# Performance work log

Hardware: AMD Instinct MI355X
Metric: run time of the kernel (lower is better)

Reference implementation:

```python
import jax, jax.numpy as jnp
import numpy as np

N = 50000
E = 800000
D = 128
NEG_SLOPE = 0.2


def _gat_layer(x, W, al, ar, b, src, dst):
    """Single-head DGL-style GATConv with ReLU activation."""
    z = x @ W                                    # [N, D] projected features
    el = z @ al                                  # [N] left attention logits
    er = z @ ar                                  # [N] right attention logits
    e = jax.nn.leaky_relu(el[src] + er[dst], NEG_SLOPE)   # [E]
    # softmax over incoming edges per destination node (numerically stable)
    m = jax.ops.segment_max(e, dst, num_segments=N)       # [N]
    ex = jnp.exp(e - m[dst])                               # [E]
    s = jax.ops.segment_sum(ex, dst, num_segments=N)       # [N]
    alpha = ex / s[dst]                                    # [E]
    out = jax.ops.segment_sum(alpha[:, None] * z[src], dst, num_segments=N)  # [N, D]
    return jax.nn.relu(out + b)


def setup_inputs() -> dict:
    key = jax.random.key(0)
    ks = jax.random.split(key, 16)
    s = 0.05
    inp = {
        "f": jax.random.normal(ks[0], (N, D), dtype=jnp.float32),
        "src": jax.random.randint(ks[1], (E,), 0, N, dtype=jnp.int32),
        "dst": jax.random.randint(ks[2], (E,), 0, N, dtype=jnp.int32),
    }
    for i, kb in zip((1, 2, 3), (3, 7, 11)):
        inp[f"W{i}"] = jax.random.normal(ks[kb], (D, D), dtype=jnp.float32) * s
        inp[f"al{i}"] = jax.random.normal(ks[kb + 1], (D,), dtype=jnp.float32) * s
        inp[f"ar{i}"] = jax.random.normal(ks[kb + 2], (D,), dtype=jnp.float32) * s
        inp[f"b{i}"] = jnp.zeros((D,), dtype=jnp.float32)
    return inp


def reference(f, src, dst, W1, al1, ar1, b1, W2, al2, ar2, b2, W3, al3, ar3, b3):
    h = _gat_layer(f, W1, al1, ar1, b1, src, dst)
    h = _gat_layer(h, W2, al2, ar2, b2, src, dst)
    h = _gat_layer(h, W3, al3, ar3, b3, src, dst)
    return h  # [N, D] (single head already squeezed)
```

## Files before the change

kernel.cpp:

```cpp
#include <hip/hip_runtime.h>
#include <hip/hip_fp16.h>
#include <math.h>

#define NN 50000
#define NE 800000
#define DD 128
#define NEG_SLOPE 0.2f
#define CAP 64
#define GBLK ((NN + 63) / 64)
#define WSBLK (3 * 16384 / 256)
#define HBLK ((NE + 255) / 256)
#define SBLK ((NE + 511) / 512)

typedef short frag8 __attribute__((ext_vector_type(8)));
typedef float f32x4 __attribute__((ext_vector_type(4)));

__device__ __forceinline__ unsigned bf16_rne(float x) {
  unsigned u = __float_as_uint(x);
  return (u + 0x7FFFu + ((u >> 16) & 1u)) >> 16;
}

__device__ __forceinline__ void wsplit_body(
    int bid, const float* __restrict__ W0, const float* __restrict__ W1,
    const float* __restrict__ W2, short* __restrict__ Wh, short* __restrict__ Wl) {
  int gidx = bid * 256 + threadIdx.x;
  int L = gidx >> 14;
  int idx = gidx & 16383;
  const float* W = (L == 0) ? W0 : (L == 1) ? W1 : W2;
  int j = idx & 7;
  int lane = (idx >> 3) & 63;
  int tile = idx >> 9;
  int nt = tile & 7, kt = tile >> 3;
  int k = kt * 32 + (lane >> 4) * 8 + j;
  int n = nt * 16 + (lane & 15);
  float x = W[k * DD + n];
  unsigned hu = bf16_rne(x);
  float hf = __uint_as_float(hu << 16);
  unsigned lu = bf16_rne(x - hf);
  Wh[gidx] = (short)hu;
  Wl[gidx] = (short)lu;
}

__device__ __forceinline__ void hist_body(int bid, const int* __restrict__ dst,
                                          int* __restrict__ deg,
                                          unsigned short* __restrict__ edge_slot) {
  int i = bid * 256 + threadIdx.x;
  if (i < NE) edge_slot[i] = (unsigned short)atomicAdd(&deg[dst[i]], 1);
}

__global__ __launch_bounds__(256) void fused_pre(
    const float* __restrict__ W0, const float* __restrict__ W1, const float* __restrict__ W2,
    short* __restrict__ Wh, short* __restrict__ Wl,
    const int* __restrict__ dst, int* __restrict__ deg,
    unsigned short* __restrict__ edge_slot) {
  if (blockIdx.x < WSBLK) wsplit_body(blockIdx.x, W0, W1, W2, Wh, Wl);
  else hist_body(blockIdx.x - WSBLK, dst, deg, edge_slot);
}

__device__ __forceinline__ void gemm_body(
    int bid, short (*sB)[8192], float (*elp)[64], float (*erp)[64],
    const float* __restrict__ x, const short* __restrict__ Wh, const short* __restrict__ Wl,
    const float* __restrict__ al, const float* __restrict__ ar,
    __half* __restrict__ z, float* __restrict__ el, float* __restrict__ er) {
  const int t = threadIdx.x;
  const int w = t >> 6, lane = t & 63;
  const int m = lane & 15, quad = lane >> 4;
  const int half = w >> 2, mw = w & 3;
  const int ntb = half * 4;
  const int R0 = bid * 64 + mw * 16;

  auto stage = [&](int kt, int buf) {
    const uint4* gh = (const uint4*)(Wh + kt * 4096);
    const uint4* gl = (const uint4*)(Wl + kt * 4096);
    uint4* s = (uint4*)sB[buf];
    s[t] = gh[t];
    s[t + 512] = gl[t];
  };

  f32x4 acc[4];
#pragma unroll
  for (int n = 0; n < 4; n++) acc[n] = (f32x4)(0.f);

  int rA = R0 + m; if (rA > NN - 1) rA = NN - 1;

  stage(0, 0);
  __syncthreads();

#pragma unroll
  for (int kt = 0; kt < 4; kt++) {
    const int buf = kt & 1;
    if (kt < 3) stage(kt + 1, buf ^ 1);

    const float* xp = x + (size_t)rA * DD + kt * 32 + quad * 8;
    float xv[8];
    *(float4*)(xv) = *(const float4*)xp;
    *(float4*)(xv + 4) = *(const float4*)(xp + 4);
    frag8 ah, alo;
#pragma unroll
    for (int j = 0; j < 8; j++) {
      unsigned hu = bf16_rne(xv[j]);
      float hf = __uint_as_float(hu << 16);
      ah[j] = (short)hu;
      alo[j] = (short)bf16_rne(xv[j] - hf);
    }
#pragma unroll
    for (int n = 0; n < 4; n++) {
      frag8 bh = *(const frag8*)&sB[buf][(ntb + n) * 512 + lane * 8];
      frag8 bl = *(const frag8*)&sB[buf][4096 + (ntb + n) * 512 + lane * 8];
      acc[n] = __builtin_amdgcn_mfma_f32_16x16x32_bf16(alo, bh, acc[n], 0, 0, 0);
      acc[n] = __builtin_amdgcn_mfma_f32_16x16x32_bf16(ah, bl, acc[n], 0, 0, 0);
      acc[n] = __builtin_amdgcn_mfma_f32_16x16x32_bf16(ah, bh, acc[n], 0, 0, 0);
    }
    __syncthreads();
  }

  float alv[4], arv[4];
#pragma unroll
  for (int n = 0; n < 4; n++) {
    alv[n] = al[(ntb + n) * 16 + m];
    arv[n] = ar[(ntb + n) * 16 + m];
  }
#pragma unroll
  for (int r = 0; r < 4; r++) {
    float pl = 0.f, pr = 0.f;
#pragma unroll
    for (int n = 0; n < 4; n++) { pl += acc[n][r] * alv[n]; pr += acc[n][r] * arv[n]; }
#pragma unroll
    for (int off = 8; off; off >>= 1) {
      pl += __shfl_xor(pl, off, 64);
      pr += __shfl_xor(pr, off, 64);
    }
    int lrow = mw * 16 + quad * 4 + r;
    if (m == 0) { elp[half][lrow] = pl; erp[half][lrow] = pr; }
    int row = R0 + quad * 4 + r;
    if (row < NN) {
#pragma unroll
      for (int n = 0; n < 4; n++) {
        unsigned short hu = __half_as_ushort(__float2half(acc[n][r]));
        unsigned short hn = (unsigned short)__shfl_xor((int)hu, 1, 64);
        if ((m & 1) == 0) {
          __half2 pair = __halves2half2(__ushort_as_half(hu), __ushort_as_half(hn));
          *(__half2*)(z + (size_t)row * DD + (ntb + n) * 16 + m) = pair;
        }
      }
    }
  }
  __syncthreads();
  if (t < 64) {
    int row = bid * 64 + t;
    if (row < NN) {
      el[row] = elp[0][t] + elp[1][t];
      er[row] = erp[0][t] + erp[1][t];
    }
  }
}

__device__ __forceinline__ void scatter_body(
    int bid, const int* __restrict__ src, const int* __restrict__ dst,
    const unsigned short* __restrict__ edge_slot, unsigned short* __restrict__ csr_src) {
  int i = bid * 512 + threadIdx.x;
  if (i >= NE) return;
  int slot = edge_slot[i]; if (slot > CAP - 1) slot = CAP - 1;
  csr_src[dst[i] * CAP + slot] = (unsigned short)src[i];
}

__global__ __launch_bounds__(512) void gemm_mfma(
    const float* __restrict__ x, const short* __restrict__ Wh, const short* __restrict__ Wl,
    const float* __restrict__ al, const float* __restrict__ ar,
    __half* __restrict__ z, float* __restrict__ el, float* __restrict__ er) {
  __shared__ __align__(16) short sB[2][8192];
  __shared__ float elp[2][64], erp[2][64];
  gemm_body(blockIdx.x, sB, elp, erp, x, Wh, Wl, al, ar, z, el, er);
}

__global__ __launch_bounds__(512) void fused_scatter_gemm(
    const float* __restrict__ x, const short* __restrict__ Wh, const short* __restrict__ Wl,
    const float* __restrict__ al, const float* __restrict__ ar,
    __half* __restrict__ z, float* __restrict__ el, float* __restrict__ er,
    const int* __restrict__ src, const int* __restrict__ dst,
    const unsigned short* __restrict__ edge_slot, unsigned short* __restrict__ csr_src) {
  __shared__ __align__(16) short sB[2][8192];
  __shared__ float elp[2][64], erp[2][64];
  if (blockIdx.x < GBLK) gemm_body(blockIdx.x, sB, elp, erp, x, Wh, Wl, al, ar, z, el, er);
  else scatter_body(blockIdx.x - GBLK, src, dst, edge_slot, csr_src);
}

__global__ __launch_bounds__(256) void gat_agg(
    const int* __restrict__ deg, const unsigned short* __restrict__ csr_src,
    const float* __restrict__ el, const float* __restrict__ er,
    const __half* __restrict__ z, const float* __restrict__ b,
    float* __restrict__ out) {
  int node = (int)((blockIdx.x * 256 + threadIdx.x) >> 6);
  int lane = threadIdx.x & 63;
  if (node >= NN) return;
  int dn = deg[node]; if (dn > CAP) dn = CAP;
  int beg = node * CAP;
  float erd = er[node];
  const __half2* zb = (const __half2*)z + lane;

  int sn = 0; float wv = 0.f;
  if (lane < dn) {
    sn = csr_src[beg + lane];
    float e = el[sn] + erd;
    e = (e > 0.f) ? e : NEG_SLOPE * e;
    wv = __expf(e);
  }
  float ssum = wv;

  float2 acc = make_float2(0.f, 0.f);
  for (int jj = 0; jj < dn; jj += 8) {
    float ww[8]; int ss[8];
#pragma unroll
    for (int u = 0; u < 8; u++) {
      ww[u] = __shfl(wv, jj + u, 64);
      ss[u] = __shfl(sn, jj + u, 64);
    }
    float2 zv[8];
#pragma unroll
    for (int u = 0; u < 8; u++) zv[u] = __half22float2(zb[(size_t)ss[u] * 64]);
#pragma unroll
    for (int u = 0; u < 8; u++) { acc.x += ww[u] * zv[u].x; acc.y += ww[u] * zv[u].y; }
  }
#pragma unroll
  for (int off = 32; off; off >>= 1) ssum += __shfl_xor(ssum, off, 64);
  float inv_s = (dn > 0) ? 1.f / ssum : 0.f;

  float2 bv = *(const float2*)(b + lane * 2);
  float ox = fmaxf(acc.x * inv_s + bv.x, 0.f);
  float oy = fmaxf(acc.y * inv_s + bv.y, 0.f);
  *(float2*)(out + (size_t)node * DD + lane * 2) = make_float2(ox, oy);
}

extern "C" void kernel_launch(void* const* d_in, const int* in_sizes, int n_in,
                              void* d_out, int out_size, void* d_ws, size_t ws_size,
                              hipStream_t stream) {
  const float* f   = (const float*)d_in[0];
  const int*   src = (const int*)d_in[1];
  const int*   dst = (const int*)d_in[2];
  const float* W[3]  = {(const float*)d_in[3], (const float*)d_in[7],  (const float*)d_in[11]};
  const float* al[3] = {(const float*)d_in[4], (const float*)d_in[8],  (const float*)d_in[12]};
  const float* ar[3] = {(const float*)d_in[5], (const float*)d_in[9],  (const float*)d_in[13]};
  const float* bb[3] = {(const float*)d_in[6], (const float*)d_in[10], (const float*)d_in[14]};

  short* Wh3 = (short*)d_ws;
  short* Wl3 = Wh3 + 3 * 16384;
  __half* zbuf = (__half*)(Wl3 + 3 * 16384);
  float* hbuf = (float*)(zbuf + (size_t)NN * DD);
  float* el = hbuf + (size_t)NN * DD;
  float* er = el + NN;
  int* deg = (int*)(er + NN);
  unsigned short* edge_slot = (unsigned short*)(deg + NN);
  unsigned short* csr_src   = edge_slot + NE;

  hipMemsetAsync(deg, 0, NN * sizeof(int), stream);
  fused_pre<<<WSBLK + HBLK, 256, 0, stream>>>(W[0], W[1], W[2], Wh3, Wl3, dst, deg, edge_slot);
  fused_scatter_gemm<<<GBLK + SBLK, 512, 0, stream>>>(f, Wh3, Wl3, al[0], ar[0],
                                                      zbuf, el, er,
                                                      src, dst, edge_slot, csr_src);
  gat_agg<<<(NN * 64) / 256, 256, 0, stream>>>(deg, csr_src, el, er, zbuf, bb[0], hbuf);

  gemm_mfma<<<GBLK, 512, 0, stream>>>(hbuf, Wh3 + 16384, Wl3 + 16384,
                                      al[1], ar[1], zbuf, el, er);
  gat_agg<<<(NN * 64) / 256, 256, 0, stream>>>(deg, csr_src, el, er, zbuf, bb[1], hbuf);

  gemm_mfma<<<GBLK, 512, 0, stream>>>(hbuf, Wh3 + 2 * 16384, Wl3 + 2 * 16384,
                                      al[2], ar[2], zbuf, el, er);
  gat_agg<<<(NN * 64) / 256, 256, 0, stream>>>(deg, csr_src, el, er, zbuf, bb[2],
                                               (float*)d_out);
}
```

Measured before the change: 290.6 us.

## Split z into column quarters and aggregate per quarter for gather locality

The projected feature buffer z is now stored as four column-quarter planes of 32 halves per node instead of row-major 128 halves. The aggregation kernel launches four block groups, one per quarter, with 16 lanes per node and 16 nodes per block. Each quarter's working set (about 3.2 MB in fp16) is more likely to stay in cache during the random source gathers. The cost is that the attention weights and softmax sums are recomputed four times, and each gather fetches only 64 bytes.

```diff
diff --git a/kernel.cpp b/kernel.cpp
--- a/kernel.cpp
+++ b/kernel.cpp
@@ -11,6 +11,7 @@
 #define WSBLK (3 * 16384 / 256)
 #define HBLK ((NE + 255) / 256)
 #define SBLK ((NE + 511) / 512)
+#define AQBLK (NN / 16)
 
 typedef short frag8 __attribute__((ext_vector_type(8)));
 typedef float f32x4 __attribute__((ext_vector_type(4)));
@@ -139,8 +140,9 @@
         unsigned short hu = __half_as_ushort(__float2half(acc[n][r]));
         unsigned short hn = (unsigned short)__shfl_xor((int)hu, 1, 64);
         if ((m & 1) == 0) {
+          int col0 = (ntb + n) * 16 + m;
           __half2 pair = __halves2half2(__ushort_as_half(hu), __ushort_as_half(hn));
-          *(__half2*)(z + (size_t)row * DD + (ntb + n) * 16 + m) = pair;
+          *(__half2*)(z + (size_t)(col0 >> 5) * NN * 32 + (size_t)row * 32 + (col0 & 31)) = pair;
         }
       }
     }
@@ -190,45 +192,60 @@
     const float* __restrict__ el, const float* __restrict__ er,
     const __half* __restrict__ z, const float* __restrict__ b,
     float* __restrict__ out) {
-  int node = (int)((blockIdx.x * 256 + threadIdx.x) >> 6);
-  int lane = threadIdx.x & 63;
-  if (node >= NN) return;
+  const int bid = blockIdx.x;
+  const int q = bid / AQBLK;
+  const int nb = bid - q * AQBLK;
+  const int t = threadIdx.x;
+  const int g = t >> 4;
+  const int l0 = t & 15;
+  const int node = nb * 16 + g;
   int dn = deg[node]; if (dn > CAP) dn = CAP;
-  int beg = node * CAP;
-  float erd = er[node];
-  const __half2* zb = (const __half2*)z + lane;
-
-  int sn = 0; float wv = 0.f;
-  if (lane < dn) {
-    sn = csr_src[beg + lane];
-    float e = el[sn] + erd;
-    e = (e > 0.f) ? e : NEG_SLOPE * e;
-    wv = __expf(e);
-  }
-  float ssum = wv;
+  const int beg = node * CAP;
+  const float erd = er[node];
+  const __half2* zq = (const __half2*)(z + (size_t)q * NN * 32) + l0;
+
+  int sn[4]; float wv[4]; float ssum = 0.f;
+#pragma unroll
+  for (int i = 0; i < 4; i++) {
+    int e = i * 16 + l0;
+    sn[i] = 0; wv[i] = 0.f;
+    if (e < dn) {
+      sn[i] = csr_src[beg + e];
+      float ev = el[sn[i]] + erd;
+      ev = (ev > 0.f) ? ev : NEG_SLOPE * ev;
+      wv[i] = __expf(ev);
+      ssum += wv[i];
+    }
+  }
+#pragma unroll
+  for (int off = 8; off; off >>= 1) ssum += __shfl_xor(ssum, off, 64);
+  float inv_s = (dn > 0) ? 1.f / ssum : 0.f;
 
   float2 acc = make_float2(0.f, 0.f);
-  for (int jj = 0; jj < dn; jj += 8) {
-    float ww[8]; int ss[8];
-#pragma unroll
-    for (int u = 0; u < 8; u++) {
-      ww[u] = __shfl(wv, jj + u, 64);
-      ss[u] = __shfl(sn, jj + u, 64);
-    }
-    float2 zv[8];
-#pragma unroll
-    for (int u = 0; u < 8; u++) zv[u] = __half22float2(zb[(size_t)ss[u] * 64]);
-#pragma unroll
-    for (int u = 0; u < 8; u++) { acc.x += ww[u] * zv[u].x; acc.y += ww[u] * zv[u].y; }
-  }
-#pragma unroll
-  for (int off = 32; off; off >>= 1) ssum += __shfl_xor(ssum, off, 64);
-  float inv_s = (dn > 0) ? 1.f / ssum : 0.f;
-
-  float2 bv = *(const float2*)(b + lane * 2);
+#pragma unroll
+  for (int i = 0; i < 4; i++) {
+    int lim = dn - i * 16;
+    if (lim <= 0) break;
+    int cnt = min(16, lim);
+    for (int jj = 0; jj < cnt; jj += 8) {
+      float ww[8]; int ss[8];
+#pragma unroll
+      for (int u = 0; u < 8; u++) {
+        ww[u] = __shfl(wv[i], g * 16 + jj + u, 64);
+        ss[u] = __shfl(sn[i], g * 16 + jj + u, 64);
+      }
+      float2 zv[8];
+#pragma unroll
+      for (int u = 0; u < 8; u++) zv[u] = __half22float2(zq[(size_t)ss[u] * 16]);
+#pragma unroll
+      for (int u = 0; u < 8; u++) { acc.x += ww[u] * zv[u].x; acc.y += ww[u] * zv[u].y; }
+    }
+  }
+
+  float2 bv = *(const float2*)(b + q * 32 + l0 * 2);
   float ox = fmaxf(acc.x * inv_s + bv.x, 0.f);
   float oy = fmaxf(acc.y * inv_s + bv.y, 0.f);
-  *(float2*)(out + (size_t)node * DD + lane * 2) = make_float2(ox, oy);
+  *(float2*)(out + (size_t)node * DD + q * 32 + l0 * 2) = make_float2(ox, oy);
 }
 
 extern "C" void kernel_launch(void* const* d_in, const int* in_sizes, int n_in,
@@ -257,14 +274,14 @@
   fused_scatter_gemm<<<GBLK + SBLK, 512, 0, stream>>>(f, Wh3, Wl3, al[0], ar[0],
                                                       zbuf, el, er,
                                                       src, dst, edge_slot, csr_src);
-  gat_agg<<<(NN * 64) / 256, 256, 0, stream>>>(deg, csr_src, el, er, zbuf, bb[0], hbuf);
+  gat_agg<<<4 * AQBLK, 256, 0, stream>>>(deg, csr_src, el, er, zbuf, bb[0], hbuf);
 
   gemm_mfma<<<GBLK, 512, 0, stream>>>(hbuf, Wh3 + 16384, Wl3 + 16384,
                                       al[1], ar[1], zbuf, el, er);
-  gat_agg<<<(NN * 64) / 256, 256, 0, stream>>>(deg, csr_src, el, er, zbuf, bb[1], hbuf);
+  gat_agg<<<4 * AQBLK, 256, 0, stream>>>(deg, csr_src, el, er, zbuf, bb[1], hbuf);
 
   gemm_mfma<<<GBLK, 512, 0, stream>>>(hbuf, Wh3 + 2 * 16384, Wl3 + 2 * 16384,
                                       al[2], ar[2], zbuf, el, er);
-  gat_agg<<<(NN * 64) / 256, 256, 0, stream>>>(deg, csr_src, el, er, zbuf, bb[2],
-                                               (float*)d_out);
-}
+  gat_agg<<<4 * AQBLK, 256, 0, stream>>>(deg, csr_src, el, er, zbuf, bb[2],
+                                         (float*)d_out);
+}
```

After: 319.7 us. +10.0%, slower.

## Load weight fragments directly from global memory instead of LDS staging

Applied to the files above, without the earlier changes.

The GEMM body no longer double-buffers the split bf16 weight tiles through shared memory with block barriers. Each wave now reads its B fragments straight from global memory, relying on L2/L1 caching of the small shared weight matrix, and all four K-slices of the input row are loaded up front. This drops the 32KB of LDS and the per-step __syncthreads, which may raise occupancy and remove barrier stalls. The cost is more global/cache traffic for the redundantly read weights and higher register pressure from holding 32 input floats per thread.

```diff
diff --git a/kernel.cpp b/kernel.cpp
--- a/kernel.cpp
+++ b/kernel.cpp
@@ -58,7 +58,7 @@
 }
 
 __device__ __forceinline__ void gemm_body(
-    int bid, short (*sB)[8192], float (*elp)[64], float (*erp)[64],
+    int bid, float (*elp)[64], float (*erp)[64],
     const float* __restrict__ x, const short* __restrict__ Wh, const short* __restrict__ Wl,
     const float* __restrict__ al, const float* __restrict__ ar,
     __half* __restrict__ z, float* __restrict__ el, float* __restrict__ er) {
@@ -69,49 +69,41 @@
   const int ntb = half * 4;
   const int R0 = bid * 64 + mw * 16;
 
-  auto stage = [&](int kt, int buf) {
-    const uint4* gh = (const uint4*)(Wh + kt * 4096);
-    const uint4* gl = (const uint4*)(Wl + kt * 4096);
-    uint4* s = (uint4*)sB[buf];
-    s[t] = gh[t];
-    s[t + 512] = gl[t];
-  };
+  int rA = R0 + m; if (rA > NN - 1) rA = NN - 1;
+
+  float xv[32];
+  const float* xp = x + (size_t)rA * DD + quad * 8;
+#pragma unroll
+  for (int i = 0; i < 4; i++) {
+    *(float4*)(xv + i * 8)     = *(const float4*)(xp + i * 32);
+    *(float4*)(xv + i * 8 + 4) = *(const float4*)(xp + i * 32 + 4);
+  }
 
   f32x4 acc[4];
 #pragma unroll
   for (int n = 0; n < 4; n++) acc[n] = (f32x4)(0.f);
 
-  int rA = R0 + m; if (rA > NN - 1) rA = NN - 1;
-
-  stage(0, 0);
-  __syncthreads();
-
 #pragma unroll
   for (int kt = 0; kt < 4; kt++) {
-    const int buf = kt & 1;
-    if (kt < 3) stage(kt + 1, buf ^ 1);
-
-    const float* xp = x + (size_t)rA * DD + kt * 32 + quad * 8;
-    float xv[8];
-    *(float4*)(xv) = *(const float4*)xp;
-    *(float4*)(xv + 4) = *(const float4*)(xp + 4);
     frag8 ah, alo;
 #pragma unroll
     for (int j = 0; j < 8; j++) {
-      unsigned hu = bf16_rne(xv[j]);
+      float xj = xv[kt * 8 + j];
+      unsigned hu = bf16_rne(xj);
       float hf = __uint_as_float(hu << 16);
       ah[j] = (short)hu;
-      alo[j] = (short)bf16_rne(xv[j] - hf);
-    }
+      alo[j] = (short)bf16_rne(xj - hf);
+    }
+    const short* bhp = Wh + kt * 4096 + ntb * 512 + lane * 8;
+    const short* blp = Wl + kt * 4096 + ntb * 512 + lane * 8;
 #pragma unroll
     for (int n = 0; n < 4; n++) {
-      frag8 bh = *(const frag8*)&sB[buf][(ntb + n) * 512 + lane * 8];
-      frag8 bl = *(const frag8*)&sB[buf][4096 + (ntb + n) * 512 + lane * 8];
+      frag8 bh = *(const frag8*)(bhp + n * 512);
+      frag8 bl = *(const frag8*)(blp + n * 512);
       acc[n] = __builtin_amdgcn_mfma_f32_16x16x32_bf16(alo, bh, acc[n], 0, 0, 0);
       acc[n] = __builtin_amdgcn_mfma_f32_16x16x32_bf16(ah, bl, acc[n], 0, 0, 0);
       acc[n] = __builtin_amdgcn_mfma_f32_16x16x32_bf16(ah, bh, acc[n], 0, 0, 0);
     }
-    __syncthreads();
   }
 
   float alv[4], arv[4];
@@ -168,9 +160,8 @@
     const float* __restrict__ x, const short* __restrict__ Wh, const short* __restrict__ Wl,
     const float* __restrict__ al, const float* __restrict__ ar,
     __half* __restrict__ z, float* __restrict__ el, float* __restrict__ er) {
-  __shared__ __align__(16) short sB[2][8192];
   __shared__ float elp[2][64], erp[2][64];
-  gemm_body(blockIdx.x, sB, elp, erp, x, Wh, Wl, al, ar, z, el, er);
+  gemm_body(blockIdx.x, elp, erp, x, Wh, Wl, al, ar, z, el, er);
 }
 
 __global__ __launch_bounds__(512) void fused_scatter_gemm(
@@ -179,9 +170,8 @@
     __half* __restrict__ z, float* __restrict__ el, float* __restrict__ er,
     const int* __restrict__ src, const int* __restrict__ dst,
     const unsigned short* __restrict__ edge_slot, unsigned short* __restrict__ csr_src) {
-  __shared__ __align__(16) short sB[2][8192];
   __shared__ float elp[2][64], erp[2][64];
-  if (blockIdx.x < GBLK) gemm_body(blockIdx.x, sB, elp, erp, x, Wh, Wl, al, ar, z, el, er);
+  if (blockIdx.x < GBLK) gemm_body(blockIdx.x, elp, erp, x, Wh, Wl, al, ar, z, el, er);
   else scatter_body(blockIdx.x - GBLK, src, dst, edge_slot, csr_src);
 }
 
```

Result: slower. 300.6 us (+3.5%).

## Fuse GAT aggregation with next layer's projection GEMM via shared memory

Applied to the files above, without the earlier changes.

Layers 1 and 2 now aggregate neighbours for 32 nodes per block and keep the ReLU'd hidden rows in shared memory. The same block then runs the next layer's split-bf16 MFMA projection and its attention logits directly from those rows. This removes the fp32 hidden-state round trip through global memory and two kernel launches, using ping-pong z/el/er buffers to avoid read-write hazards. In exchange, the GEMM phase uses smaller 32-row tiles that read B fragments straight from global memory, and the aggregation and GEMM phases can no longer overlap across blocks as well.

```diff
diff --git a/kernel.cpp b/kernel.cpp
--- a/kernel.cpp
+++ b/kernel.cpp
@@ -11,6 +11,7 @@
 #define WSBLK (3 * 16384 / 256)
 #define HBLK ((NE + 255) / 256)
 #define SBLK ((NE + 511) / 512)
+#define AGBLK ((NN + 31) / 32)
 
 typedef short frag8 __attribute__((ext_vector_type(8)));
 typedef float f32x4 __attribute__((ext_vector_type(4)));
@@ -164,15 +165,6 @@
   csr_src[dst[i] * CAP + slot] = (unsigned short)src[i];
 }
 
-__global__ __launch_bounds__(512) void gemm_mfma(
-    const float* __restrict__ x, const short* __restrict__ Wh, const short* __restrict__ Wl,
-    const float* __restrict__ al, const float* __restrict__ ar,
-    __half* __restrict__ z, float* __restrict__ el, float* __restrict__ er) {
-  __shared__ __align__(16) short sB[2][8192];
-  __shared__ float elp[2][64], erp[2][64];
-  gemm_body(blockIdx.x, sB, elp, erp, x, Wh, Wl, al, ar, z, el, er);
-}
-
 __global__ __launch_bounds__(512) void fused_scatter_gemm(
     const float* __restrict__ x, const short* __restrict__ Wh, const short* __restrict__ Wl,
     const float* __restrict__ al, const float* __restrict__ ar,
@@ -185,6 +177,143 @@
   else scatter_body(blockIdx.x - GBLK, src, dst, edge_slot, csr_src);
 }
 
+__device__ __forceinline__ float2 agg_node(
+    int node, int lane, const int* __restrict__ deg,
+    const unsigned short* __restrict__ csr_src, const float* __restrict__ el,
+    float erd, const __half* __restrict__ z, float* inv_s_out) {
+  int dn = deg[node]; if (dn > CAP) dn = CAP;
+  int beg = node * CAP;
+  const __half2* zb = (const __half2*)z + lane;
+
+  int sn = 0; float wv = 0.f;
+  if (lane < dn) {
+    sn = csr_src[beg + lane];
+    float e = el[sn] + erd;
+    e = (e > 0.f) ? e : NEG_SLOPE * e;
+    wv = __expf(e);
+  }
+  float ssum = wv;
+
+  float2 acc = make_float2(0.f, 0.f);
+  for (int jj = 0; jj < dn; jj += 8) {
+    float ww[8]; int ss[8];
+#pragma unroll
+    for (int u = 0; u < 8; u++) {
+      ww[u] = __shfl(wv, jj + u, 64);
+      ss[u] = __shfl(sn, jj + u, 64);
+    }
+    float2 zv[8];
+#pragma unroll
+    for (int u = 0; u < 8; u++) zv[u] = __half22float2(zb[(size_t)ss[u] * 64]);
+#pragma unroll
+    for (int u = 0; u < 8; u++) { acc.x += ww[u] * zv[u].x; acc.y += ww[u] * zv[u].y; }
+  }
+#pragma unroll
+  for (int off = 32; off; off >>= 1) ssum += __shfl_xor(ssum, off, 64);
+  *inv_s_out = (dn > 0) ? 1.f / ssum : 0.f;
+  return acc;
+}
+
+__global__ __launch_bounds__(512) void agg_gemm(
+    const int* __restrict__ deg, const unsigned short* __restrict__ csr_src,
+    const float* __restrict__ el_in, const float* __restrict__ er_in,
+    const __half* __restrict__ z_in, const float* __restrict__ bias,
+    const short* __restrict__ Wh, const short* __restrict__ Wl,
+    const float* __restrict__ al, const float* __restrict__ ar,
+    __half* __restrict__ z_out, float* __restrict__ el_out, float* __restrict__ er_out) {
+  __shared__ __align__(16) float hS[32][132];
+  __shared__ float elp[4][32], erp[4][32];
+
+  const int t = threadIdx.x;
+  const int w = t >> 6, lane = t & 63;
+  const int R0 = blockIdx.x * 32;
+
+  float2 bv = *(const float2*)(bias + lane * 2);
+#pragma unroll 1
+  for (int u = 0; u < 4; u++) {
+    int lrow = w * 4 + u;
+    int node = R0 + lrow;
+    float hx = 0.f, hy = 0.f;
+    if (node < NN) {
+      float inv_s;
+      float2 acc = agg_node(node, lane, deg, csr_src, el_in, er_in[node], z_in, &inv_s);
+      hx = fmaxf(acc.x * inv_s + bv.x, 0.f);
+      hy = fmaxf(acc.y * inv_s + bv.y, 0.f);
+    }
+    *(float2*)&hS[lrow][lane * 2] = make_float2(hx, hy);
+  }
+  __syncthreads();
+
+  const int m = lane & 15, quad = lane >> 4;
+  const int mt = w >> 2, p = w & 3;
+  const int nt0 = p, nt1 = p + 4;
+  f32x4 acc0 = (f32x4)(0.f), acc1 = (f32x4)(0.f);
+
+#pragma unroll
+  for (int kt = 0; kt < 4; kt++) {
+    const float* hp = &hS[mt * 16 + m][kt * 32 + quad * 8];
+    float xv[8];
+    *(float4*)(xv) = *(const float4*)hp;
+    *(float4*)(xv + 4) = *(const float4*)(hp + 4);
+    frag8 ah, alo;
+#pragma unroll
+    for (int j = 0; j < 8; j++) {
+      unsigned hu = bf16_rne(xv[j]);
+      float hf = __uint_as_float(hu << 16);
+      ah[j] = (short)hu;
+      alo[j] = (short)bf16_rne(xv[j] - hf);
+    }
+    const short* bhp = Wh + kt * 4096 + lane * 8;
+    const short* blp = Wl + kt * 4096 + lane * 8;
+    frag8 bh0 = *(const frag8*)(bhp + nt0 * 512);
+    frag8 bl0 = *(const frag8*)(blp + nt0 * 512);
+    frag8 bh1 = *(const frag8*)(bhp + nt1 * 512);
+    frag8 bl1 = *(const frag8*)(blp + nt1 * 512);
+    acc0 = __builtin_amdgcn_mfma_f32_16x16x32_bf16(alo, bh0, acc0, 0, 0, 0);
+    acc0 = __builtin_amdgcn_mfma_f32_16x16x32_bf16(ah, bl0, acc0, 0, 0, 0);
+    acc0 = __builtin_amdgcn_mfma_f32_16x16x32_bf16(ah, bh0, acc0, 0, 0, 0);
+    acc1 = __builtin_amdgcn_mfma_f32_16x16x32_bf16(alo, bh1, acc1, 0, 0, 0);
+    acc1 = __builtin_amdgcn_mfma_f32_16x16x32_bf16(ah, bl1, acc1, 0, 0, 0);
+    acc1 = __builtin_amdgcn_mfma_f32_16x16x32_bf16(ah, bh1, acc1, 0, 0, 0);
+  }
+
+  float alv0 = al[nt0 * 16 + m], arv0 = ar[nt0 * 16 + m];
+  float alv1 = al[nt1 * 16 + m], arv1 = ar[nt1 * 16 + m];
+#pragma unroll
+  for (int r = 0; r < 4; r++) {
+    float pl = acc0[r] * alv0 + acc1[r] * alv1;
+    float pr = acc0[r] * arv0 + acc1[r] * arv1;
+#pragma unroll
+    for (int off = 8; off; off >>= 1) {
+      pl += __shfl_xor(pl, off, 64);
+      pr += __shfl_xor(pr, off, 64);
+    }
+    int lrow = mt * 16 + quad * 4 + r;
+    if (m == 0) { elp[p][lrow] = pl; erp[p][lrow] = pr; }
+    int row = R0 + lrow;
+    if (row < NN) {
+      unsigned short hu0 = __half_as_ushort(__float2half(acc0[r]));
+      unsigned short hn0 = (unsigned short)__shfl_xor((int)hu0, 1, 64);
+      unsigned short hu1 = __half_as_ushort(__float2half(acc1[r]));
+      unsigned short hn1 = (unsigned short)__shfl_xor((int)hu1, 1, 64);
+      if ((m & 1) == 0) {
+        *(__half2*)(z_out + (size_t)row * DD + nt0 * 16 + m) =
+            __halves2half2(__ushort_as_half(hu0), __ushort_as_half(hn0));
+        *(__half2*)(z_out + (size_t)row * DD + nt1 * 16 + m) =
+            __halves2half2(__ushort_as_half(hu1), __ushort_as_half(hn1));
+      }
+    }
+  }
+  __syncthreads();
+  if (t < 32) {
+    int row = R0 + t;
+    if (row < NN) {
+      el_out[row] = elp[0][t] + elp[1][t] + elp[2][t] + elp[3][t];
+      er_out[row] = erp[0][t] + erp[1][t] + erp[2][t] + erp[3][t];
+    }
+  }
+}
+
 __global__ __launch_bounds__(256) void gat_agg(
     const int* __restrict__ deg, const unsigned short* __restrict__ csr_src,
     const float* __restrict__ el, const float* __restrict__ er,
@@ -193,41 +322,11 @@
   int node = (int)((blockIdx.x * 256 + threadIdx.x) >> 6);
   int lane = threadIdx.x & 63;
   if (node >= NN) return;
-  int dn = deg[node]; if (dn > CAP) dn = CAP;
-  int beg = node * CAP;
-  float erd = er[node];
-  const __half2* zb = (const __half2*)z + lane;
-
-  int sn = 0; float wv = 0.f;
-  if (lane < dn) {
-    sn = csr_src[beg + lane];
-    float e = el[sn] + erd;
-    e = (e > 0.f) ? e : NEG_SLOPE * e;
-    wv = __expf(e);
-  }
-  float ssum = wv;
-
-  float2 acc = make_float2(0.f, 0.f);
-  for (int jj = 0; jj < dn; jj += 8) {
-    float ww[8]; int ss[8];
-#pragma unroll
-    for (int u = 0; u < 8; u++) {
-      ww[u] = __shfl(wv, jj + u, 64);
-      ss[u] = __shfl(sn, jj + u, 64);
-    }
-    float2 zv[8];
-#pragma unroll
-    for (int u = 0; u < 8; u++) zv[u] = __half22float2(zb[(size_t)ss[u] * 64]);
-#pragma unroll
-    for (int u = 0; u < 8; u++) { acc.x += ww[u] * zv[u].x; acc.y += ww[u] * zv[u].y; }
-  }
-#pragma unroll
-  for (int off = 32; off; off >>= 1) ssum += __shfl_xor(ssum, off, 64);
-  float inv_s = (dn > 0) ? 1.f / ssum : 0.f;
-
-  float2 bv = *(const float2*)(b + lane * 2);
-  float ox = fmaxf(acc.x * inv_s + bv.x, 0.f);
-  float oy = fmaxf(acc.y * inv_s + bv.y, 0.f);
+  float inv_s;
+  float2 acc = agg_node(node, lane, deg, csr_src, el, er[node], z, &inv_s);
+  float2 bvv = *(const float2*)(b + lane * 2);
+  float ox = fmaxf(acc.x * inv_s + bvv.x, 0.f);
+  float oy = fmaxf(acc.y * inv_s + bvv.y, 0.f);
   *(float2*)(out + (size_t)node * DD + lane * 2) = make_float2(ox, oy);
 }
 
@@ -244,27 +343,27 @@
 
   short* Wh3 = (short*)d_ws;
   short* Wl3 = Wh3 + 3 * 16384;
-  __half* zbuf = (__half*)(Wl3 + 3 * 16384);
-  float* hbuf = (float*)(zbuf + (size_t)NN * DD);
-  float* el = hbuf + (size_t)NN * DD;
-  float* er = el + NN;
-  int* deg = (int*)(er + NN);
+  __half* zA = (__half*)(Wl3 + 3 * 16384);
+  __half* zB = zA + (size_t)NN * DD;
+  float* el  = (float*)(zB + (size_t)NN * DD);
+  float* er  = el + NN;
+  float* el2 = er + NN;
+  float* er2 = el2 + NN;
+  int* deg = (int*)(er2 + NN);
   unsigned short* edge_slot = (unsigned short*)(deg + NN);
   unsigned short* csr_src   = edge_slot + NE;
 
   hipMemsetAsync(deg, 0, NN * sizeof(int), stream);
   fused_pre<<<WSBLK + HBLK, 256, 0, stream>>>(W[0], W[1], W[2], Wh3, Wl3, dst, deg, edge_slot);
   fused_scatter_gemm<<<GBLK + SBLK, 512, 0, stream>>>(f, Wh3, Wl3, al[0], ar[0],
-                                                      zbuf, el, er,
+                                                      zA, el, er,
                                                       src, dst, edge_slot, csr_src);
-  gat_agg<<<(NN * 64) / 256, 256, 0, stream>>>(deg, csr_src, el, er, zbuf, bb[0], hbuf);
-
-  gemm_mfma<<<GBLK, 512, 0, stream>>>(hbuf, Wh3 + 16384, Wl3 + 16384,
-                                      al[1], ar[1], zbuf, el, er);
-  gat_agg<<<(NN * 64) / 256, 256, 0, stream>>>(deg, csr_src, el, er, zbuf, bb[1], hbuf);
-
-  gemm_mfma<<<GBLK, 512, 0, stream>>>(hbuf, Wh3 + 2 * 16384, Wl3 + 2 * 16384,
-                                      al[2], ar[2], zbuf, el, er);
-  gat_agg<<<(NN * 64) / 256, 256, 0, stream>>>(deg, csr_src, el, er, zbuf, bb[2],
+  agg_gemm<<<AGBLK, 512, 0, stream>>>(deg, csr_src, el, er, zA, bb[0],
+                                      Wh3 + 16384, Wl3 + 16384, al[1], ar[1],
+                                      zB, el2, er2);
+  agg_gemm<<<AGBLK, 512, 0, stream>>>(deg, csr_src, el2, er2, zB, bb[1],
+                                      Wh3 + 2 * 16384, Wl3 + 2 * 16384, al[2], ar[2],
+                                      zA, el, er);
+  gat_agg<<<(NN * 64) / 256, 256, 0, stream>>>(deg, csr_src, el, er, zA, bb[2],
                                                (float*)d_out);
 }
```

Result: faster. 283.3 us (-2.5%).
